# Optimization experiments

Measured on AMD Instinct MI355X. Metric: run time of the kernel, lower is better.

Reference implementation:

```python
import jax, jax.numpy as jnp
import numpy as np
import math

C = 32  # per-head channel dim (init arg c)


def _layernorm(x, g, b, eps=1e-5):
    mu = x.mean(-1, keepdims=True)
    var = ((x - mu) ** 2).mean(-1, keepdims=True)
    return (x - mu) * jax.lax.rsqrt(var + eps) * g + b


def setup_inputs() -> dict:
    key = jax.random.key(0)
    ks = jax.random.split(key, 8)
    S, N, D = 17, 4096, 256  # S = 1 target + 16 MSTA templates
    h = jax.random.normal(ks[0], (S, N, D), jnp.float32)
    msta_mask = jax.random.uniform(ks[1], (S - 1, N)) < 0.5
    # module requires count(target_msta_mask) == count(msta_mask); use equal masks
    target_msta_mask = msta_mask
    w = lambda k: jax.random.normal(k, (D, D), jnp.float32) * 0.05
    return dict(
        h=h, target_msta_mask=target_msta_mask, msta_mask=msta_mask,
        Wq=w(ks[2]), Wk=w(ks[3]), Wv=w(ks[4]), Wo=w(ks[5]),
        bo=jnp.zeros((D,), jnp.float32),
        ln_g=jnp.ones((D,), jnp.float32), ln_b=jnp.zeros((D,), jnp.float32),
    )


def reference(h, target_msta_mask, msta_mask, Wq, Wk, Wv, Wo, bo, ln_g, ln_b):
    S, N, D = h.shape
    H = D // C
    M = msta_mask.shape[0]  # == S - 1
    # --- msta_h[target_msta_mask] = h[1:][msta_mask] (rank-matched scatter, jit-safe) ---
    h1 = h[1:].reshape(M * N, D)
    src = msta_mask.reshape(-1)
    dst = target_msta_mask.reshape(-1)
    src_rank = jnp.cumsum(src.astype(jnp.int32)) - 1
    buf = jnp.zeros((M * N, D), h.dtype).at[jnp.where(src, src_rank, M * N)].set(h1, mode='drop')
    dst_rank = jnp.clip(jnp.cumsum(dst.astype(jnp.int32)) - 1, 0, M * N - 1)
    msta_h = jnp.where(dst[:, None], buf[dst_rank], 0.0).reshape(M, N, D)
    # --- full-column equivalent of the subset attention (per-position independent) ---
    cols = target_msta_mask.any(0)                      # [N]
    attn_h = jnp.concatenate([h[:1], msta_h], axis=0)   # [S, N, D]
    mask = jnp.concatenate([cols[None], target_msta_mask], axis=0)  # [S, N]; == inverse_mask == attn_mask (full cols)
    q = (attn_h @ Wq.T).reshape(S, N, H, C)
    k = (attn_h @ Wk.T).reshape(S, N, H, C)
    v = (attn_h @ Wv.T).reshape(S, N, H, C)
    att = jnp.einsum('snhc,tnhc->stnh', q, k) / math.sqrt(C)
    att = att - (~mask).astype(h.dtype)[None, :, :, None] * 1e9
    att = jax.nn.softmax(att, axis=1)                   # softmax over key-sample axis t
    attn_o = jnp.einsum('stnh,tnhc->snhc', att, v).reshape(S, N, D)
    # o[inverse_mask] = attn_o[attn_mask]  (masks coincide in full-column form)
    o = jnp.where(mask[..., None], attn_o, h @ Wv.T)
    o = o @ Wo.T + bo
    # dropout is identity in eval mode
    return _layernorm(h + o, ln_g, ln_b)
```

## Files before the change

kernel.cpp:

```cpp
#include <hip/hip_runtime.h>
#include <hip/hip_bf16.h>

#define S 17
#define NPOS 4096
#define D 256
#define NH 8
#define CH 32
#define MROWS 16

typedef __attribute__((ext_vector_type(8))) short bf16x8;
typedef __attribute__((ext_vector_type(4))) float f32x4;

__device__ __forceinline__ float bfu(unsigned short u) {
  return __uint_as_float(((unsigned int)u) << 16);
}
__device__ __forceinline__ unsigned short f2b(float f) {
  __hip_bfloat16 t = __float2bfloat16(f);
  return *reinterpret_cast<unsigned short*>(&t);
}
__device__ __forceinline__ void unpack16(const uint4 A, const uint4 B, float* r) {
  r[0]  = __uint_as_float(A.x << 16); r[1]  = __uint_as_float(A.x & 0xffff0000u);
  r[2]  = __uint_as_float(A.y << 16); r[3]  = __uint_as_float(A.y & 0xffff0000u);
  r[4]  = __uint_as_float(A.z << 16); r[5]  = __uint_as_float(A.z & 0xffff0000u);
  r[6]  = __uint_as_float(A.w << 16); r[7]  = __uint_as_float(A.w & 0xffff0000u);
  r[8]  = __uint_as_float(B.x << 16); r[9]  = __uint_as_float(B.x & 0xffff0000u);
  r[10] = __uint_as_float(B.y << 16); r[11] = __uint_as_float(B.y & 0xffff0000u);
  r[12] = __uint_as_float(B.z << 16); r[13] = __uint_as_float(B.z & 0xffff0000u);
  r[14] = __uint_as_float(B.w << 16); r[15] = __uint_as_float(B.w & 0xffff0000u);
}
__device__ __forceinline__ float readv(const void* p, int f32, size_t i) {
  return f32 ? ((const float*)p)[i] : bfu(((const unsigned short*)p)[i]);
}

__device__ __forceinline__ void gl_lds16(const unsigned short* g, unsigned short* l) {
  __builtin_amdgcn_global_load_lds(
      (const __attribute__((address_space(1))) unsigned int*)g,
      (__attribute__((address_space(3))) unsigned int*)l, 16, 0, 0);
}

struct TensorList {
  const unsigned short* p[8];
  int n[8];
};

__global__ void detect_multi_kernel(TensorList tl, int* __restrict__ flags) {
  __shared__ int s_totnz, s_evnz, s_evwild;
  if (threadIdx.x == 0) { s_totnz = 0; s_evnz = 0; s_evwild = 0; }
  __syncthreads();
  const unsigned short* p = tl.p[blockIdx.x];
  const int n = tl.n[blockIdx.x];
  const int w = n < 4096 ? n : 4096;
  int totnz = 0, evnz = 0, evwild = 0;
  for (int i = threadIdx.x; i < w; i += blockDim.x) {
    unsigned short u = p[i];
    if (u) {
      totnz++;
      if (!(i & 1)) {
        evnz++;
        int e = (u >> 7) & 0xFF;
        if (e == 0 || e == 255 || e < 97 || e > 157) evwild++;
      }
    }
  }
  atomicAdd(&s_totnz, totnz);
  atomicAdd(&s_evnz, evnz);
  atomicAdd(&s_evwild, evwild);
  __syncthreads();
  if (threadIdx.x == 0) {
    const int evcount = w / 2;
    int f;
    if (s_totnz == 0) f = 0;
    else if (s_evnz == 0) f = 1;
    else if (s_evwild * 8 > evcount) f = 1;
    else f = 0;
    flags[blockIdx.x] = f;
  }
}

__global__ void detect_mask_kernel(const unsigned int* __restrict__ w,
                                   int* __restrict__ cls) {
  __shared__ int viol[5];
  if (threadIdx.x < 5) viol[threadIdx.x] = 0;
  __syncthreads();
  int v_i32 = 0, v_f32 = 0, v_bf16 = 0, v_u8 = 0, v_i64 = 0;
  const int nwords = 65536 / 4;
  for (int i = threadIdx.x; i < nwords; i += blockDim.x) {
    unsigned int x = w[i];
    if (x > 1u) v_i32 = 1;
    if (x != 0u && x != 0x3F800000u) v_f32 = 1;
    unsigned int lo = x & 0xFFFFu, hi = x >> 16;
    if ((lo != 0u && lo != 0x3F80u) || (hi != 0u && hi != 0x3F80u)) v_bf16 = 1;
    if ((x & 0xFEFEFEFEu) != 0u) v_u8 = 1;
    if ((i & 1) && x != 0u) v_i64 = 1;
  }
  if (v_i32) atomicOr(&viol[0], 1);
  if (v_f32) atomicOr(&viol[1], 1);
  if (v_bf16) atomicOr(&viol[2], 1);
  if (v_u8) atomicOr(&viol[3], 1);
  if (v_i64) atomicOr(&viol[4], 1);
  __syncthreads();
  if (threadIdx.x == 0) {
    int c;
    if (!viol[0] && !viol[4]) c = 4;
    else if (!viol[0]) c = 0;
    else if (!viol[1]) c = 2;
    else if (!viol[2]) c = 3;
    else c = 1;
    *cls = c;
  }
}

__global__ void expand_mask_kernel(const void* __restrict__ tmask, const int* __restrict__ cls,
                                   unsigned char* __restrict__ mask_u8) {
  int n = blockIdx.x * blockDim.x + threadIdx.x;
  if (n >= NPOS) return;
  const int c = *cls;
  int any = 0;
  for (int m = 0; m < MROWS; m++) {
    size_t idx = (size_t)m * NPOS + n;
    int v;
    if (c == 0)      v = ((const int*)tmask)[idx] != 0;
    else if (c == 1) v = ((const unsigned char*)tmask)[idx] != 0;
    else if (c == 2) v = ((const unsigned int*)tmask)[idx] != 0u;
    else if (c == 3) v = ((const unsigned short*)tmask)[idx] != 0u;
    else             v = ((const unsigned long long*)tmask)[idx] != 0ull;
    mask_u8[(m + 1) * NPOS + n] = (unsigned char)v;
    any |= v;
  }
  mask_u8[n] = (unsigned char)any;
}

struct WPtrs { const void* p[4]; };

__global__ void conv_w_kernel(WPtrs wp, const int* __restrict__ flags,
                              unsigned short* __restrict__ w_bf) {
  for (int i = blockIdx.x * blockDim.x + threadIdx.x; i < 4 * 65536;
       i += gridDim.x * blockDim.x) {
    int which = i >> 16, off = i & 65535;
    int f = flags[1 + which];
    w_bf[i] = f ? f2b(((const float*)wp.p[which])[off])
                : ((const unsigned short*)wp.p[which])[off];
  }
}

__global__ __launch_bounds__(256) void qkv_kernel(
    const void* __restrict__ h, const int* __restrict__ flags,
    const unsigned short* __restrict__ w_bf,
    unsigned short* __restrict__ q_ws, unsigned short* __restrict__ k_ws,
    unsigned short* __restrict__ v_ws) {
  __shared__ unsigned short lds[16384];
  const int tid = threadIdx.x;
  const int wave = tid >> 6, lane = tid & 63;
  const int l15 = lane & 15, quad = lane >> 4;
  const int bid = blockIdx.x;
  const int nt = bid % 6;
  const size_t mt = bid / 6;
  const size_t R = mt * 128;
  const unsigned short* Wb = w_bf + (size_t)(nt * 128) * 256;
  const int hf32 = flags[0];
  const int srow = lane >> 3;
  const int scol = (lane & 7) * 8;
  const int wm = wave >> 1, wn = wave & 1;

  f32x4 acc[4][4];
  #pragma unroll
  for (int a = 0; a < 4; a++)
    #pragma unroll
    for (int b = 0; b < 4; b++) acc[a][b] = (f32x4){0.f, 0.f, 0.f, 0.f};

  for (int k0 = 0; k0 < 4; k0++) {
    if (hf32) {
      const float* hf = (const float*)h;
      #pragma unroll
      for (int i = 0; i < 4; i++) {
        int row = i * 32 + wave * 8 + srow;
        const float4* src = (const float4*)&hf[(R + row) * 256 + k0 * 64 + scol];
        float4 v0 = src[0], v1 = src[1];
        unsigned int w0 = ((unsigned)f2b(v0.y) << 16) | f2b(v0.x);
        unsigned int w1 = ((unsigned)f2b(v0.w) << 16) | f2b(v0.z);
        unsigned int w2 = ((unsigned)f2b(v1.y) << 16) | f2b(v1.x);
        unsigned int w3 = ((unsigned)f2b(v1.w) << 16) | f2b(v1.z);
        *(uint4*)&lds[i * 2048 + wave * 512 + lane * 8] = make_uint4(w0, w1, w2, w3);
      }
    } else {
      const unsigned short* hb = (const unsigned short*)h;
      #pragma unroll
      for (int i = 0; i < 4; i++) {
        int row = i * 32 + wave * 8 + srow;
        gl_lds16(&hb[(R + row) * 256 + k0 * 64 + scol], &lds[i * 2048 + wave * 512]);
      }
    }
    #pragma unroll
    for (int i = 0; i < 4; i++) {
      int row = i * 32 + wave * 8 + srow;
      gl_lds16(&Wb[(size_t)row * 256 + k0 * 64 + scol], &lds[8192 + i * 2048 + wave * 512]);
    }
    asm volatile("s_waitcnt vmcnt(0)" ::: "memory");
    __syncthreads();
    bf16x8 af[4][2], bfr[4][2];
    #pragma unroll
    for (int mi = 0; mi < 4; mi++)
      #pragma unroll
      for (int kk = 0; kk < 2; kk++)
        af[mi][kk] = *(const bf16x8*)&lds[(wm * 64 + mi * 16 + l15) * 64 + kk * 32 + quad * 8];
    #pragma unroll
    for (int ni = 0; ni < 4; ni++)
      #pragma unroll
      for (int kk = 0; kk < 2; kk++)
        bfr[ni][kk] = *(const bf16x8*)&lds[8192 + (wn * 64 + ni * 16 + l15) * 64 + kk * 32 + quad * 8];
    #pragma unroll
    for (int kk = 0; kk < 2; kk++)
      #pragma unroll
      for (int mi = 0; mi < 4; mi++)
        #pragma unroll
        for (int ni = 0; ni < 4; ni++)
          acc[mi][ni] = __builtin_amdgcn_mfma_f32_16x16x32_bf16(af[mi][kk], bfr[ni][kk],
                                                                acc[mi][ni], 0, 0, 0);
    __syncthreads();
  }
  const int p = nt >> 1;
  const int cbase = (nt & 1) * 128;
  unsigned short* dst = (p == 0) ? q_ws : (p == 1) ? k_ws : v_ws;
  #pragma unroll
  for (int mi = 0; mi < 4; mi++)
    #pragma unroll
    for (int ni = 0; ni < 4; ni++)
      #pragma unroll
      for (int r = 0; r < 4; r++) {
        int row = wm * 64 + mi * 16 + quad * 4 + r;
        int col = cbase + wn * 64 + ni * 16 + l15;
        dst[(R + row) * 256 + col] = f2b(acc[mi][ni][r]);
      }
}

__global__ __launch_bounds__(256) void attn_kernel(
    const unsigned short* __restrict__ q_ws, const unsigned short* __restrict__ k_ws,
    const unsigned short* __restrict__ v_ws, const unsigned char* __restrict__ mask_u8,
    unsigned short* __restrict__ o_ws) {
  __shared__ unsigned short qb[S * D], kb[S * D], vb[S * D];
  __shared__ float pmat[S * 160];
  __shared__ unsigned char sm[32];
  const int tid = threadIdx.x;
  const int n = blockIdx.x;
  if (tid < S) sm[tid] = mask_u8[tid * NPOS + n];
  for (int idx = tid; idx < S * 32; idx += 256) {
    int s = idx >> 5, c = idx & 31;
    size_t g = ((size_t)s * NPOS + n) * 32 + c;
    ((uint4*)qb)[idx] = ((const uint4*)q_ws)[g];
    ((uint4*)kb)[idx] = ((const uint4*)k_ws)[g];
    ((uint4*)vb)[idx] = ((const uint4*)v_ws)[g];
  }
  __syncthreads();
  {
    const int hh = tid >> 5, s = tid & 31;
    if (s < S) {
      float qv[32];
      const uint4* qp = (const uint4*)(qb + s * 256 + hh * 32);
      unpack16(qp[0], qp[1], qv);
      unpack16(qp[2], qp[3], qv + 16);
      const float scale = 0.17677669529663687f;
      float sc[S];
      float mx = -3.4e38f;
      #pragma unroll
      for (int t = 0; t < S; t++) {
        const uint4* kp = (const uint4*)(kb + t * 256 + hh * 32);
        float kv[16];
        unpack16(kp[0], kp[1], kv);
        float a = 0.f;
        #pragma unroll
        for (int u = 0; u < 16; u++) a = fmaf(qv[u], kv[u], a);
        unpack16(kp[2], kp[3], kv);
        #pragma unroll
        for (int u = 0; u < 16; u++) a = fmaf(qv[16 + u], kv[u], a);
        a *= scale;
        if (!sm[t]) a -= 1e9f;
        sc[t] = a;
        mx = fmaxf(mx, a);
      }
      float sum = 0.f;
      #pragma unroll
      for (int t = 0; t < S; t++) { sc[t] = __expf(sc[t] - mx); sum += sc[t]; }
      const float inv = 1.f / sum;
      float* pr = pmat + s * 160 + hh * 20;
      #pragma unroll
      for (int t = 0; t < S; t++) pr[t] = sc[t] * inv;
      pr[17] = 0.f; pr[18] = 0.f; pr[19] = 0.f;
    }
  }
  __syncthreads();
  {
    const int d = tid, hh = d >> 5;
    float vf[S];
    #pragma unroll
    for (int t = 0; t < S; t++) vf[t] = bfu(vb[t * 256 + d]);
    #pragma unroll 1
    for (int s = 0; s < S; s++) {
      const float* pr = pmat + s * 160 + hh * 20;
      float ov = 0.f;
      #pragma unroll
      for (int t = 0; t < S; t++) ov = fmaf(pr[t], vf[t], ov);
      const float o_val = sm[s] ? ov : vf[s];
      o_ws[((size_t)s * NPOS + n) * 256 + d] = f2b(o_val);
    }
  }
}

template <int HF32>
__device__ __forceinline__ void oproj_body(
    const unsigned short* __restrict__ o_ws, const void* __restrict__ h,
    const unsigned short* __restrict__ w_bf, const int* __restrict__ fl,
    const void* __restrict__ bo, const void* __restrict__ lng,
    const void* __restrict__ lnb, float* __restrict__ out,
    unsigned short* As) {
  const int tid = threadIdx.x;
  const size_t R = (size_t)blockIdx.x * 128;
  for (int idx = tid; idx < 128 * 32; idx += 256) {
    int r = idx >> 5, c = idx & 31;
    *(uint4*)&As[r * 264 + c * 8] = ((const uint4*)o_ws)[(R + r) * 32 + c];
  }
  __syncthreads();
  const int wave = tid >> 6, lane = tid & 63;
  const int l15 = lane & 15, quad = lane >> 4;
  bf16x8 af0[8], af1[8];
  #pragma unroll
  for (int t = 0; t < 8; t++) {
    af0[t] = *(const bf16x8*)&As[(wave * 32 + l15) * 264 + t * 32 + quad * 8];
    af1[t] = *(const bf16x8*)&As[(wave * 32 + 16 + l15) * 264 + t * 32 + quad * 8];
  }
  const unsigned short* Wp = w_bf + 3 * 65536;
  f32x4 acc0[16], acc1[16];
  #pragma unroll
  for (int j = 0; j < 16; j++) {
    acc0[j] = (f32x4){0.f, 0.f, 0.f, 0.f};
    acc1[j] = (f32x4){0.f, 0.f, 0.f, 0.f};
  }
  #pragma unroll
  for (int t = 0; t < 8; t++) {
    #pragma unroll
    for (int j = 0; j < 16; j++) {
      bf16x8 b = *(const bf16x8*)(Wp + (j * 16 + l15) * 256 + t * 32 + quad * 8);
      acc0[j] = __builtin_amdgcn_mfma_f32_16x16x32_bf16(af0[t], b, acc0[j], 0, 0, 0);
      acc1[j] = __builtin_amdgcn_mfma_f32_16x16x32_bf16(af1[t], b, acc1[j], 0, 0, 0);
    }
  }
  const int f5 = fl[5], f6 = fl[6], f7 = fl[7];
  float xsum0[4] = {0, 0, 0, 0}, xsq0[4] = {0, 0, 0, 0};
  float xsum1[4] = {0, 0, 0, 0}, xsq1[4] = {0, 0, 0, 0};
  #pragma unroll
  for (int j = 0; j < 16; j++) {
    const int col = j * 16 + l15;
    const float boj = readv(bo, f5, col);
    #pragma unroll
    for (int r = 0; r < 4; r++) {
      const size_t row0 = R + wave * 32 + quad * 4 + r;
      const size_t row1 = row0 + 16;
      float h0 = HF32 ? ((const float*)h)[row0 * 256 + col]
                      : bfu(((const unsigned short*)h)[row0 * 256 + col]);
      float h1 = HF32 ? ((const float*)h)[row1 * 256 + col]
                      : bfu(((const unsigned short*)h)[row1 * 256 + col]);
      float x0 = acc0[j][r] + h0 + boj;
      float x1 = acc1[j][r] + h1 + boj;
      acc0[j][r] = x0; acc1[j][r] = x1;
      xsum0[r] += x0; xsq0[r] += x0 * x0;
      xsum1[r] += x1; xsq1[r] += x1 * x1;
    }
  }
  #pragma unroll
  for (int r = 0; r < 4; r++) {
    #pragma unroll
    for (int m = 1; m <= 8; m <<= 1) {
      xsum0[r] += __shfl_xor(xsum0[r], m, 64);
      xsq0[r]  += __shfl_xor(xsq0[r], m, 64);
      xsum1[r] += __shfl_xor(xsum1[r], m, 64);
      xsq1[r]  += __shfl_xor(xsq1[r], m, 64);
    }
  }
  float mu0[4], rs0[4], mu1[4], rs1[4];
  #pragma unroll
  for (int r = 0; r < 4; r++) {
    mu0[r] = xsum0[r] * (1.0f / 256.0f);
    rs0[r] = rsqrtf(fmaxf(xsq0[r] * (1.0f / 256.0f) - mu0[r] * mu0[r], 0.0f) + 1e-5f);
    mu1[r] = xsum1[r] * (1.0f / 256.0f);
    rs1[r] = rsqrtf(fmaxf(xsq1[r] * (1.0f / 256.0f) - mu1[r] * mu1[r], 0.0f) + 1e-5f);
  }
  #pragma unroll
  for (int j = 0; j < 16; j++) {
    const int col = j * 16 + l15;
    const float gj = readv(lng, f6, col);
    const float bj = readv(lnb, f7, col);
    #pragma unroll
    for (int r = 0; r < 4; r++) {
      const size_t row0 = R + wave * 32 + quad * 4 + r;
      out[row0 * 256 + col] = (acc0[j][r] - mu0[r]) * rs0[r] * gj + bj;
      out[(row0 + 16) * 256 + col] = (acc1[j][r] - mu1[r]) * rs1[r] * gj + bj;
    }
  }
}

__global__ __launch_bounds__(256) void oproj_ln_kernel(
    const unsigned short* __restrict__ o_ws, const void* __restrict__ h,
    const unsigned short* __restrict__ w_bf, const int* __restrict__ flags,
    const void* __restrict__ bo, const void* __restrict__ lng,
    const void* __restrict__ lnb, float* __restrict__ out) {
  __shared__ unsigned short As[128 * 264];
  if (flags[0]) oproj_body<1>(o_ws, h, w_bf, flags, bo, lng, lnb, out, As);
  else          oproj_body<0>(o_ws, h, w_bf, flags, bo, lng, lnb, out, As);
}

extern "C" void kernel_launch(void* const* d_in, const int* in_sizes, int n_in,
                              void* d_out, int out_size, void* d_ws, size_t ws_size,
                              hipStream_t stream) {
  const void* h     = d_in[0];
  const void* tmask = d_in[1];
  const void* Wq  = d_in[3];
  const void* Wk  = d_in[4];
  const void* Wv  = d_in[5];
  const void* Wo  = d_in[6];
  const void* bo  = d_in[7];
  const void* lng = d_in[8];
  const void* lnb = d_in[9];
  float* out = (float*)d_out;

  char* ws = (char*)d_ws;
  int* mcls  = (int*)ws;
  int* flags = (int*)(ws + 64);
  unsigned char* mask_u8 = (unsigned char*)(ws + 4096);
  unsigned short* w_bf = (unsigned short*)(ws + 73728);
  unsigned short* q_ws = (unsigned short*)(ws + 598016);
  unsigned short* k_ws = (unsigned short*)(ws + 598016 + 35651584ull);
  unsigned short* v_ws = (unsigned short*)(ws + 598016 + 2 * 35651584ull);
  unsigned short* o_ws = q_ws;

  TensorList tl;
  tl.p[0] = (const unsigned short*)h;   tl.n[0] = in_sizes[0];
  tl.p[1] = (const unsigned short*)Wq;  tl.n[1] = in_sizes[3];
  tl.p[2] = (const unsigned short*)Wk;  tl.n[2] = in_sizes[4];
  tl.p[3] = (const unsigned short*)Wv;  tl.n[3] = in_sizes[5];
  tl.p[4] = (const unsigned short*)Wo;  tl.n[4] = in_sizes[6];
  tl.p[5] = (const unsigned short*)bo;  tl.n[5] = in_sizes[7];
  tl.p[6] = (const unsigned short*)lng; tl.n[6] = in_sizes[8];
  tl.p[7] = (const unsigned short*)lnb; tl.n[7] = in_sizes[9];
  WPtrs wp;
  wp.p[0] = Wq; wp.p[1] = Wk; wp.p[2] = Wv; wp.p[3] = Wo;

  detect_multi_kernel<<<8, 256, 0, stream>>>(tl, flags);
  detect_mask_kernel<<<1, 256, 0, stream>>>((const unsigned int*)tmask, mcls);
  expand_mask_kernel<<<NPOS / 256, 256, 0, stream>>>(tmask, mcls, mask_u8);
  conv_w_kernel<<<256, 256, 0, stream>>>(wp, flags, w_bf);
  qkv_kernel<<<544 * 6, 256, 0, stream>>>(h, flags, w_bf, q_ws, k_ws, v_ws);
  attn_kernel<<<NPOS, 256, 0, stream>>>(q_ws, k_ws, v_ws, mask_u8, o_ws);
  oproj_ln_kernel<<<S * NPOS / 128, 256, 0, stream>>>(o_ws, h, w_bf, flags,
                                                      bo, lng, lnb, out);
}
```

Baseline: 425.8 us.

## Stage O-projection A and Wo tiles through LDS with direct global-to-LDS loads

The output-projection GEMM now loops over K in chunks of 64. Each chunk loads both the activation tile and the Wo weight tile into LDS using global-to-LDS copies, where before the activations were staged in LDS and the weights were read straight from global memory for every MFMA. The goal is to cut repeated global and L2 traffic for Wo and to shrink the LDS footprint from about 66KB to 48KB, which may raise occupancy. In exchange it adds two barriers per K chunk with no double buffering, and the unpadded 64-wide LDS rows may cause bank conflicts.

```diff
diff --git a/kernel.cpp b/kernel.cpp
--- a/kernel.cpp
+++ b/kernel.cpp
@@ -311,38 +311,52 @@
     const unsigned short* __restrict__ w_bf, const int* __restrict__ fl,
     const void* __restrict__ bo, const void* __restrict__ lng,
     const void* __restrict__ lnb, float* __restrict__ out,
-    unsigned short* As) {
+    unsigned short* lds) {
   const int tid = threadIdx.x;
-  const size_t R = (size_t)blockIdx.x * 128;
-  for (int idx = tid; idx < 128 * 32; idx += 256) {
-    int r = idx >> 5, c = idx & 31;
-    *(uint4*)&As[r * 264 + c * 8] = ((const uint4*)o_ws)[(R + r) * 32 + c];
-  }
-  __syncthreads();
   const int wave = tid >> 6, lane = tid & 63;
   const int l15 = lane & 15, quad = lane >> 4;
-  bf16x8 af0[8], af1[8];
-  #pragma unroll
-  for (int t = 0; t < 8; t++) {
-    af0[t] = *(const bf16x8*)&As[(wave * 32 + l15) * 264 + t * 32 + quad * 8];
-    af1[t] = *(const bf16x8*)&As[(wave * 32 + 16 + l15) * 264 + t * 32 + quad * 8];
-  }
+  const int srow = lane >> 3;
+  const int scol = (lane & 7) * 8;
+  const size_t R = (size_t)blockIdx.x * 128;
   const unsigned short* Wp = w_bf + 3 * 65536;
+
   f32x4 acc0[16], acc1[16];
   #pragma unroll
   for (int j = 0; j < 16; j++) {
     acc0[j] = (f32x4){0.f, 0.f, 0.f, 0.f};
     acc1[j] = (f32x4){0.f, 0.f, 0.f, 0.f};
   }
-  #pragma unroll
-  for (int t = 0; t < 8; t++) {
-    #pragma unroll
-    for (int j = 0; j < 16; j++) {
-      bf16x8 b = *(const bf16x8*)(Wp + (j * 16 + l15) * 256 + t * 32 + quad * 8);
-      acc0[j] = __builtin_amdgcn_mfma_f32_16x16x32_bf16(af0[t], b, acc0[j], 0, 0, 0);
-      acc1[j] = __builtin_amdgcn_mfma_f32_16x16x32_bf16(af1[t], b, acc1[j], 0, 0, 0);
-    }
-  }
+
+  for (int k0 = 0; k0 < 4; k0++) {
+    #pragma unroll
+    for (int i = 0; i < 4; i++) {
+      int row = i * 32 + wave * 8 + srow;
+      gl_lds16(&o_ws[(R + row) * 256 + k0 * 64 + scol], &lds[i * 2048 + wave * 512]);
+    }
+    #pragma unroll
+    for (int i = 0; i < 8; i++) {
+      int row = i * 32 + wave * 8 + srow;
+      gl_lds16(&Wp[(size_t)row * 256 + k0 * 64 + scol], &lds[8192 + i * 2048 + wave * 512]);
+    }
+    asm volatile("s_waitcnt vmcnt(0)" ::: "memory");
+    __syncthreads();
+    bf16x8 af0k[2], af1k[2];
+    #pragma unroll
+    for (int kk = 0; kk < 2; kk++) {
+      af0k[kk] = *(const bf16x8*)&lds[(wave * 32 + l15) * 64 + kk * 32 + quad * 8];
+      af1k[kk] = *(const bf16x8*)&lds[(wave * 32 + 16 + l15) * 64 + kk * 32 + quad * 8];
+    }
+    #pragma unroll
+    for (int kk = 0; kk < 2; kk++)
+      #pragma unroll
+      for (int j = 0; j < 16; j++) {
+        bf16x8 b = *(const bf16x8*)&lds[8192 + (j * 16 + l15) * 64 + kk * 32 + quad * 8];
+        acc0[j] = __builtin_amdgcn_mfma_f32_16x16x32_bf16(af0k[kk], b, acc0[j], 0, 0, 0);
+        acc1[j] = __builtin_amdgcn_mfma_f32_16x16x32_bf16(af1k[kk], b, acc1[j], 0, 0, 0);
+      }
+    __syncthreads();
+  }
+
   const int f5 = fl[5], f6 = fl[6], f7 = fl[7];
   float xsum0[4] = {0, 0, 0, 0}, xsq0[4] = {0, 0, 0, 0};
   float xsum1[4] = {0, 0, 0, 0}, xsq1[4] = {0, 0, 0, 0};
@@ -402,9 +416,9 @@
     const unsigned short* __restrict__ w_bf, const int* __restrict__ flags,
     const void* __restrict__ bo, const void* __restrict__ lng,
     const void* __restrict__ lnb, float* __restrict__ out) {
-  __shared__ unsigned short As[128 * 264];
-  if (flags[0]) oproj_body<1>(o_ws, h, w_bf, flags, bo, lng, lnb, out, As);
-  else          oproj_body<0>(o_ws, h, w_bf, flags, bo, lng, lnb, out, As);
+  __shared__ unsigned short lds[24576];
+  if (flags[0]) oproj_body<1>(o_ws, h, w_bf, flags, bo, lng, lnb, out, lds);
+  else          oproj_body<0>(o_ws, h, w_bf, flags, bo, lng, lnb, out, lds);
 }
 
 extern "C" void kernel_launch(void* const* d_in, const int* in_sizes, int n_in,
```

After: 392.7 us. 7.8% less time.
